# Kernel tuning notes

Hardware: AMD Instinct MI355X
Metric: run time of the kernel (lower is better)

The kernel has to match this reference:

```python
import jax, jax.numpy as jnp
import numpy as np

ALPHA = 4.0  # spikingjelly surrogate.Sigmoid default
TAU = 2.0    # LIFNode default

@jax.custom_vjp
def spike(x):
    return (x >= 0).astype(x.dtype)

def _spike_fwd(x):
    return spike(x), x

def _spike_bwd(x, g):
    s = jax.nn.sigmoid(ALPHA * x)
    return (g * ALPHA * s * (1.0 - s),)

spike.defvjp(_spike_fwd, _spike_bwd)

def lif(x_seq, v_th):
    # multi-step LIF over leading time dim; decay_input=True, v_reset=0 (hard reset)
    def step(v, x):
        v = v + (x - v) / TAU
        s = spike(v - v_th)
        return v * (1.0 - s), s
    _, s_seq = jax.lax.scan(step, jnp.zeros_like(x_seq[0]), x_seq)
    return s_seq

def bn_c(x, gamma, beta, mean, var, eps=1e-5):
    # eval-mode BatchNorm1d over channel axis 2 of [T,N,C,V]
    inv = (gamma / jnp.sqrt(var + eps))[None, None, :, None]
    return (x - mean[None, None, :, None]) * inv + beta[None, None, :, None]

def conv1x1(x, w):
    # 1x1 Conv1d == channel mixing: w [Cout,Cin], x [T,N,C,V]
    return jnp.einsum('oc,tncv->tnov', w, x)

def setup_inputs() -> dict:
    key = jax.random.key(0)
    T, N, C, V = 4, 512, 256, 25
    ks = jax.random.split(key, 24)
    def bn_params(k1, k2, k3, k4):
        return (jax.random.uniform(k1, (C,)) * 0.5 + 0.75,
                jax.random.normal(k2, (C,)) * 0.1,
                jax.random.normal(k3, (C,)) * 0.1,
                jax.random.uniform(k4, (C,)) * 0.5 + 0.5)
    x = jax.random.normal(ks[0], (T, N, C, V), dtype=jnp.float32)
    s = 1.0 / np.sqrt(C)
    wq = jax.random.normal(ks[1], (C, C)) * s
    wk = jax.random.normal(ks[2], (C, C)) * s
    wv = jax.random.normal(ks[3], (C, C)) * s
    wp = jax.random.normal(ks[4], (C, C)) * s
    bp = jax.random.normal(ks[5], (C,)) * 0.02
    qg, qb, qm, qvar = bn_params(ks[6], ks[7], ks[8], ks[9])
    kg, kb, km, kvar = bn_params(ks[10], ks[11], ks[12], ks[13])
    vg, vb, vm, vvar = bn_params(ks[14], ks[15], ks[16], ks[17])
    pg, pb, pm, pvar = bn_params(ks[18], ks[19], ks[20], ks[21])
    return dict(x=x, wq=wq, wk=wk, wv=wv, wp=wp, bp=bp,
                qg=qg, qb=qb, qm=qm, qvar=qvar,
                kg=kg, kb=kb, km=km, kvar=kvar,
                vg=vg, vb=vb, vm=vm, vvar=vvar,
                pg=pg, pb=pb, pm=pm, pvar=pvar)

def reference(x, wq, wk, wv, wp, bp, qg, qb, qm, qvar, kg, kb, km, kvar,
              vg, vb, vm, vvar, pg, pb, pm, pvar):
    T, N, C, V = x.shape
    H = 8
    D = C // H
    scale = 0.125

    def branch(w, g, b, m, var):
        s = lif(bn_c(conv1x1(x, w), g, b, m, var), 1.0)       # [T,N,C,V]
        # -> [T,N,V,C] -> [T,N,V,H,D] -> [T,N,H,V,D]
        return jnp.transpose(s, (0, 1, 3, 2)).reshape(T, N, V, H, D).transpose(0, 1, 3, 2, 4)

    q = branch(wq, qg, qb, qm, qvar)
    k = branch(wk, kg, kb, km, kvar)
    v = branch(wv, vg, vb, vm, vvar)

    attn = jnp.einsum('tnhvd,tnhwd->tnhvw', q, k)            # binary spike attn, no softmax
    y = jnp.einsum('tnhvw,tnhwd->tnhvd', attn, v) * scale    # [T,N,H,V,D]
    y = y.transpose(0, 1, 2, 4, 3).reshape(T, N, C, V)       # transpose(3,4) then merge H*D=C
    y = lif(y, 0.5)                                          # attn_lif, v_threshold=0.5
    y = conv1x1(y, wp) + bp[None, None, :, None]             # proj_conv (bias=True)
    y = lif(bn_c(y, pg, pb, pm, pvar), 1.0)                  # proj_bn + proj_lif
    return y + x                                             # residual
```

## Files before the change

### kernel.cpp

```cpp
#include <hip/hip_runtime.h>
#include <cstdint>
#include <cstddef>

#define T_ 4
#define N_ 512
#define C_ 256
#define V_ 25
#define H_ 8

typedef _Float16 half8_t __attribute__((ext_vector_type(8)));
typedef float f32x16 __attribute__((ext_vector_type(16)));

__device__ __forceinline__ f32x16 mfma16(half8_t a, half8_t b, f32x16 c) {
  return __builtin_amdgcn_mfma_f32_32x32x16_f16(a, b, c, 0, 0, 0);
}

__global__ void kw_stage(const float* __restrict__ wq, const float* __restrict__ wk,
                         const float* __restrict__ wv, const float* __restrict__ wp,
                         const float* __restrict__ qg, const float* __restrict__ qvar,
                         const float* __restrict__ kg, const float* __restrict__ kvar,
                         const float* __restrict__ vg, const float* __restrict__ vvar,
                         const float* __restrict__ pg, const float* __restrict__ pvar,
                         _Float16* __restrict__ Wstg) {
  int i = blockIdx.x * 512 + threadIdx.x;
  int j = i & 7, lane = (i >> 3) & 63, rt = (i >> 9) & 3, m = (i >> 11) & 1;
  int s = (i >> 12) & 3, p = (i >> 14) & 3, c = i >> 16;
  int kt = p * 4 + s;
  int row = rt * 32 + (lane & 31);
  int k = kt * 16 + (lane >> 5) * 8 + j;
  const float *w, *g, *va;
  int grow;
  if (c < 6) {
    int br = c >> 1;
    w = br == 0 ? wq : br == 1 ? wk : wv;
    g = br == 0 ? qg : br == 1 ? kg : vg;
    va = br == 0 ? qvar : br == 1 ? kvar : vvar;
    grow = (c & 1) * 128 + row;
  } else {
    w = wp; g = pg; va = pvar;
    grow = (c - 6) * 128 + row;
  }
  float sc = g[grow] / sqrtf(va[grow] + 1e-5f);
  float wv_ = w[grow * 256 + k] * sc;
  _Float16 hi = (_Float16)wv_;
  Wstg[i] = (m == 0) ? hi : (_Float16)(wv_ - (float)hi);
}

__global__ void kx_stage(const float* __restrict__ x, _Float16* __restrict__ X16) {
  __shared__ float Xt[256 * 28];
  const int n = blockIdx.x, tid = threadIdx.x;
  for (int t = 0; t < 4; ++t) {
    __syncthreads();
    for (int i = tid; i < 6400; i += 256) {
      int k = i / 25, v = i - k * 25;
      Xt[k * 28 + v] = x[(size_t)(t * N_ + n) * 6400 + i];
    }
    __syncthreads();
    for (int jj = tid; jj < 800; jj += 256) {
      int kt = jj / 50, r = jj - kt * 50;
      int v = r >> 1, lkg = r & 1;
      int k0 = kt * 16 + lkg * 8;
      half8_t hi, lo;
#pragma unroll
      for (int e = 0; e < 8; ++e) {
        float f = Xt[(k0 + e) * 28 + v];
        _Float16 h = (_Float16)f;
        hi[e] = h;
        lo[e] = (_Float16)(f - (float)h);
      }
      int col = v * 4 + t;
      size_t base = (size_t)(n * 2) * 25600 + kt * 1600 + col * 16 + lkg * 8;
      *(half8_t*)(X16 + base) = hi;
      *(half8_t*)(X16 + base + 25600) = lo;
    }
  }
}

#define STAGE_A(gidx, bufsel)                                                     \
  do {                                                                            \
    const _Float16* sp_ = Wstg + (size_t)(gidx) * 16384 + tid * 8;                \
    char* dp_ = Abuf + (bufsel) * 32768 + tid * 16;                               \
    __builtin_amdgcn_global_load_lds((const uint32_t*)(sp_),          (uint32_t*)(dp_),          16, 0, 0); \
    __builtin_amdgcn_global_load_lds((const uint32_t*)(sp_ + 4096),   (uint32_t*)(dp_ + 8192),   16, 0, 0); \
    __builtin_amdgcn_global_load_lds((const uint32_t*)(sp_ + 8192),   (uint32_t*)(dp_ + 16384),  16, 0, 0); \
    __builtin_amdgcn_global_load_lds((const uint32_t*)(sp_ + 12288),  (uint32_t*)(dp_ + 24576),  16, 0, 0); \
  } while (0)

#define MS_BYTE(colx, rowx) ((colx) * 256 + (((rowx) * 4) ^ (((colx) & 7) << 4)))

__global__ __launch_bounds__(512, 1) void k1d(
    const _Float16* __restrict__ X16, const _Float16* __restrict__ Wstg,
    const float* __restrict__ qg, const float* __restrict__ qb,
    const float* __restrict__ qm, const float* __restrict__ qvar,
    const float* __restrict__ kg, const float* __restrict__ kb,
    const float* __restrict__ km, const float* __restrict__ kvar,
    const float* __restrict__ vg, const float* __restrict__ vb,
    const float* __restrict__ vm, const float* __restrict__ vvar,
    uint32_t* __restrict__ masks) {
  __shared__ __align__(16) char LDSb[65536 + 51200 + 3072];
  char* Abuf = LDSb;
  char* MsB = LDSb + 65536;
  float* bicL = (float*)(LDSb + 65536 + 51200);

  const int np = blockIdx.x, tid = threadIdx.x;
  const int lane = tid & 63, wid = tid >> 6;
  const int rg = wid & 1, cg = wid >> 1;
  const int lr = lane & 31, lkg = lane >> 5;

  for (int i = tid; i < 768; i += 512) {
    int cc = i >> 7, row = i & 127;
    int br = cc >> 1, ch = (cc & 1) * 128 + row;
    const float* g  = br == 0 ? qg : br == 1 ? kg : vg;
    const float* be = br == 0 ? qb : br == 1 ? kb : vb;
    const float* mu = br == 0 ? qm : br == 1 ? km : vm;
    const float* va = br == 0 ? qvar : br == 1 ? kvar : vvar;
    float sc = g[ch] / sqrtf(va[ch] + 1e-5f);
    bicL[i] = be[ch] - mu[ch] * sc;
  }

  const int colw0 = cg * 64 + lr, colw1 = cg * 64 + 32 + lr;
  int c0 = colw0 > 199 ? 199 : colw0, c1 = colw1 > 199 ? 199 : colw1;
  int nl0 = (c0 >= 100), cl0 = c0 - nl0 * 100;
  int nl1 = (c1 >= 100), cl1 = c1 - nl1 * 100;
  const _Float16* xh0 = X16 + (size_t)((np * 2 + nl0) * 2 + 0) * 25600 + cl0 * 16 + lkg * 8;
  const _Float16* xl0 = X16 + (size_t)((np * 2 + nl0) * 2 + 1) * 25600 + cl0 * 16 + lkg * 8;
  const _Float16* xh1 = X16 + (size_t)((np * 2 + nl1) * 2 + 0) * 25600 + cl1 * 16 + lkg * 8;
  const _Float16* xl1 = X16 + (size_t)((np * 2 + nl1) * 2 + 1) * 25600 + cl1 * 16 + lkg * 8;

  STAGE_A(0, 0);
  half8_t Bh0[2], Bh1[2], Bl0[2], Bl1[2];
  Bh0[0] = *(const half8_t*)(xh0);
  Bh1[0] = *(const half8_t*)(xh1);
  Bl0[0] = *(const half8_t*)(xl0);
  Bl1[0] = *(const half8_t*)(xl1);

  for (int c = 0; c < 6; ++c) {
    const int br = c >> 1;
    f32x16 acc00 = {}, acc01 = {}, acc10 = {}, acc11 = {};
#pragma unroll
    for (int p = 0; p < 4; ++p) {
      __syncthreads();
      int gnext = c * 4 + p + 1;
      if (gnext < 24) STAGE_A(gnext, (p + 1) & 1);
#pragma unroll
      for (int s = 0; s < 4; ++s) {
        const int kt = p * 4 + s;
        const int cur = kt & 1, nxt = cur ^ 1;
        const int ktn = ((kt + 1) & 15) * 1600;
        Bh0[nxt] = *(const half8_t*)(xh0 + ktn);
        Bh1[nxt] = *(const half8_t*)(xh1 + ktn);
        Bl0[nxt] = *(const half8_t*)(xl0 + ktn);
        Bl1[nxt] = *(const half8_t*)(xl1 + ktn);
        const char* base = Abuf + (p & 1) * 32768 + s * 8192 + (rg * 2) * 1024 + lane * 16;
        half8_t Ah0 = *(const half8_t*)(base);
        half8_t Ah1 = *(const half8_t*)(base + 1024);
        half8_t Al0 = *(const half8_t*)(base + 4096);
        half8_t Al1 = *(const half8_t*)(base + 4096 + 1024);
        __builtin_amdgcn_s_setprio(1);
        acc00 = mfma16(Ah0, Bh0[cur], acc00);
        acc01 = mfma16(Ah0, Bh1[cur], acc01);
        acc10 = mfma16(Ah1, Bh0[cur], acc10);
        acc11 = mfma16(Ah1, Bh1[cur], acc11);
        acc00 = mfma16(Ah0, Bl0[cur], acc00);
        acc01 = mfma16(Ah0, Bl1[cur], acc01);
        acc10 = mfma16(Ah1, Bl0[cur], acc10);
        acc11 = mfma16(Ah1, Bl1[cur], acc11);
        acc00 = mfma16(Al0, Bh0[cur], acc00);
        acc01 = mfma16(Al0, Bh1[cur], acc01);
        acc10 = mfma16(Al1, Bh0[cur], acc10);
        acc11 = mfma16(Al1, Bh1[cur], acc11);
        __builtin_amdgcn_s_setprio(0);
      }
    }

#pragma unroll
    for (int pp = 0; pp < 2; ++pp) {
      __syncthreads();
      if (rg == pp) {
#pragma unroll
        for (int sub = 0; sub < 2; ++sub) {
#pragma unroll
          for (int ct = 0; ct < 2; ++ct) {
            int col = ct ? colw1 : colw0;
            if (col < 200) {
              f32x16 A = sub ? (ct ? acc11 : acc10) : (ct ? acc01 : acc00);
#pragma unroll
              for (int qq = 0; qq < 4; ++qq) {
                int rowb = sub * 32 + qq * 8 + lkg * 4;
                *(float4*)(MsB + MS_BYTE(col, rowb)) =
                    make_float4(A[qq * 4], A[qq * 4 + 1], A[qq * 4 + 2], A[qq * 4 + 3]);
              }
            }
          }
        }
      }
      __syncthreads();
      const int d = lane & 31, hl = lane >> 5;
      for (int it = 0; it < 7; ++it) {
        int task = it * 16 + wid * 2 + hl;
        bool valid = task < 100;
        int tnl = valid ? task / 50 : 0;
        int r = valid ? task - tnl * 50 : 0;
        int hgl = r / 25, v = r - (r / 25) * 25;
        int row = hgl * 32 + d;
        float bicv = bicL[c * 128 + pp * 64 + row];
        float st = 0.0f;
#pragma unroll
        for (int t = 0; t < 4; ++t) {
          int colx = tnl * 100 + v * 4 + t;
          float cu = *(const float*)(MsB + MS_BYTE(colx, row)) + bicv;
          st += (cu - st) * 0.5f;
          bool sb = valid && (st >= 1.0f);
          if (st >= 1.0f) st = 0.0f;
          unsigned long long b = __ballot(sb);
          if (valid && (lane == 0 || lane == 32)) {
            uint32_t wd = (lane == 0) ? (uint32_t)b : (uint32_t)(b >> 32);
            int hg = (c & 1) * 4 + pp * 2 + hgl;
            int n = np * 2 + tnl;
            masks[((((size_t)t * N_ + n) * 3 + br) * H_ + hg) * V_ + v] = wd;
          }
        }
      }
    }
  }
}

__launch_bounds__(64)
__global__ void k2_attn(const uint32_t* __restrict__ masks, uint32_t* __restrict__ mask2) {
  __shared__ uint32_t qs[T_][V_], ks_[T_][V_], vs[T_][V_];
  const int n = blockIdx.x >> 3;
  const int h = blockIdx.x & 7;
  const int l = threadIdx.x;
  for (int i = l; i < T_ * 3 * V_; i += 64) {
    int t = i / (3 * V_);
    int r = i - t * (3 * V_);
    int br = r / V_;
    int v = r - br * V_;
    uint32_t w = masks[(((size_t)t * N_ + n) * 3 + br) * (H_ * V_) + h * V_ + v];
    if (br == 0) qs[t][v] = w;
    else if (br == 1) ks_[t][v] = w;
    else vs[t][v] = w;
  }
  __syncthreads();
  const int hi = l >> 5, d = l & 31;
  float st[13];
#pragma unroll
  for (int vv = 0; vv < 13; ++vv) st[vv] = 0.0f;
#pragma unroll
  for (int t = 0; t < 4; ++t) {
    uint32_t q[13];
    int y[13];
#pragma unroll
    for (int vv = 0; vv < 13; ++vv) {
      int v = vv * 2 + hi;
      q[vv] = qs[t][v < V_ ? v : 0];
      y[vv] = 0;
    }
    for (int w = 0; w < V_; ++w) {
      uint32_t kw = ks_[t][w];
      int vb = (int)((vs[t][w] >> d) & 1u);
#pragma unroll
      for (int vv = 0; vv < 13; ++vv) y[vv] += __popc(q[vv] & kw) * vb;
    }
#pragma unroll
    for (int vv = 0; vv < 13; ++vv) {
      int v = vv * 2 + hi;
      bool valid = (v < V_);
      float yf = 0.125f * (float)y[vv];
      st[vv] += (yf - st[vv]) * 0.5f;
      bool s = valid && (st[vv] >= 0.5f);
      if (st[vv] >= 0.5f) st[vv] = 0.0f;
      unsigned long long b = __ballot(s);
      if (valid && (l == 0 || l == 32)) {
        uint32_t wd = (l == 0) ? (uint32_t)b : (uint32_t)(b >> 32);
        mask2[(((size_t)t * N_ + n) * V_ + v) * H_ + h] = wd;
      }
    }
  }
}

__global__ __launch_bounds__(512, 1) void k3d(
    const float* __restrict__ x, const _Float16* __restrict__ Wstg,
    const uint32_t* __restrict__ mask2, const float* __restrict__ bp,
    const float* __restrict__ pg, const float* __restrict__ pb,
    const float* __restrict__ pm, const float* __restrict__ pvar,
    float* __restrict__ out) {
  __shared__ __align__(16) char LDSb[65536 + 51200 + 1024 + 6400];
  char* Abuf = LDSb;
  char* MsB = LDSb + 65536;
  float* bicL = (float*)(LDSb + 65536 + 51200);
  uint32_t* m2s = (uint32_t*)(LDSb + 65536 + 51200 + 1024);

  const int np = blockIdx.x, tid = threadIdx.x;
  const int lane = tid & 63, wid = tid >> 6;
  const int rg = wid & 1, cg = wid >> 1;
  const int lr = lane & 31, lkg = lane >> 5;

  for (int i = tid; i < 1600; i += 512) {
    int nl = i / 800, j = i - nl * 800;
    int t = j / 200, r = j - t * 200;
    m2s[i] = mask2[(size_t)(t * N_ + np * 2 + nl) * 200 + r];
  }
  if (tid < 256) {
    float sc = pg[tid] / sqrtf(pvar[tid] + 1e-5f);
    bicL[tid] = fmaf(bp[tid] - pm[tid], sc, pb[tid]);
  }
  __syncthreads();

  const int colw0 = cg * 64 + lr, colw1 = cg * 64 + 32 + lr;
  int c0 = colw0 > 199 ? 199 : colw0, c1 = colw1 > 199 ? 199 : colw1;
  int nl0 = (c0 >= 100), cl0 = c0 - nl0 * 100;
  int nl1 = (c1 >= 100), cl1 = c1 - nl1 * 100;
  const int v0 = cl0 >> 2, t0 = cl0 & 3, v1 = cl1 >> 2, t1 = cl1 & 3;
  const int mb0 = nl0 * 800 + t0 * 200 + v0 * 8;
  const int mb1 = nl1 * 800 + t1 * 200 + v1 * 8;

  STAGE_A(24, 0);
  for (int c = 0; c < 2; ++c) {
    f32x16 acc00 = {}, acc01 = {}, acc10 = {}, acc11 = {};
#pragma unroll
    for (int p = 0; p < 4; ++p) {
      __syncthreads();
      int gnext = 24 + c * 4 + p + 1;
      if (gnext < 32) STAGE_A(gnext, (p + 1) & 1);
#pragma unroll
      for (int s = 0; s < 4; ++s) {
        const int kt = p * 4 + s;
        uint32_t w0 = m2s[mb0 + (kt >> 1)];
        uint32_t w1 = m2s[mb1 + (kt >> 1)];
        int sh = (kt & 1) * 16 + lkg * 8;
        half8_t B0, B1;
#pragma unroll
        for (int jj = 0; jj < 8; ++jj) {
          B0[jj] = ((w0 >> (sh + jj)) & 1u) ? (_Float16)1.0f : (_Float16)0.0f;
          B1[jj] = ((w1 >> (sh + jj)) & 1u) ? (_Float16)1.0f : (_Float16)0.0f;
        }
        const char* base = Abuf + (p & 1) * 32768 + s * 8192 + (rg * 2) * 1024 + lane * 16;
        half8_t Ah0 = *(const half8_t*)(base);
        half8_t Ah1 = *(const half8_t*)(base + 1024);
        half8_t Al0 = *(const half8_t*)(base + 4096);
        half8_t Al1 = *(const half8_t*)(base + 4096 + 1024);
        __builtin_amdgcn_s_setprio(1);
        acc00 = mfma16(Ah0, B0, acc00);
        acc01 = mfma16(Ah0, B1, acc01);
        acc10 = mfma16(Ah1, B0, acc10);
        acc11 = mfma16(Ah1, B1, acc11);
        acc00 = mfma16(Al0, B0, acc00);
        acc01 = mfma16(Al0, B1, acc01);
        acc10 = mfma16(Al1, B0, acc10);
        acc11 = mfma16(Al1, B1, acc11);
        __builtin_amdgcn_s_setprio(0);
      }
    }

#pragma unroll
    for (int pp = 0; pp < 2; ++pp) {
      __syncthreads();
      if (rg == pp) {
#pragma unroll
        for (int sub = 0; sub < 2; ++sub) {
#pragma unroll
          for (int ct = 0; ct < 2; ++ct) {
            int col = ct ? colw1 : colw0;
            if (col < 200) {
              f32x16 A = sub ? (ct ? acc11 : acc10) : (ct ? acc01 : acc00);
#pragma unroll
              for (int qq = 0; qq < 4; ++qq) {
                int rowb = sub * 32 + qq * 8 + lkg * 4;
                *(float4*)(MsB + MS_BYTE(col, rowb)) =
                    make_float4(A[qq * 4], A[qq * 4 + 1], A[qq * 4 + 2], A[qq * 4 + 3]);
              }
            }
          }
        }
      }
      __syncthreads();
      {
        const int d = lane & 31, hl = lane >> 5;
        for (int it = 0; it < 7; ++it) {
          int task = it * 16 + wid * 2 + hl;
          bool valid = task < 100;
          int tnl = valid ? task / 50 : 0;
          int r = valid ? task - tnl * 50 : 0;
          int hgl = r / 25, v = r - (r / 25) * 25;
          int row = hgl * 32 + d;
          float bicv = bicL[c * 128 + pp * 64 + row];
          float st = 0.0f;
#pragma unroll
          for (int t = 0; t < 4; ++t) {
            int colx = tnl * 100 + v * 4 + t;
            char* mp = MsB + MS_BYTE(colx, row);
            if (valid) {
              float cu = *(const float*)(mp) + bicv;
              st += (cu - st) * 0.5f;
              float sv = (st >= 1.0f) ? 1.0f : 0.0f;
              if (st >= 1.0f) st = 0.0f;
              *(float*)(mp) = sv;
            }
          }
        }
      }
      __syncthreads();
      for (int ii = tid; ii < 12800; ii += 512) {
        int t = ii / 3200, r = ii - t * 3200;
        int nl = r / 1600, r2 = r - nl * 1600;
        int cl = r2 / 25, v = r2 - cl * 25;
        int colx = nl * 100 + v * 4 + t;
        float sv = *(const float*)(MsB + MS_BYTE(colx, cl));
        size_t go = (size_t)(t * N_ + np * 2 + nl) * 6400 +
                    (size_t)(c * 128 + pp * 64 + cl) * 25 + v;
        out[go] = sv + x[go];
      }
    }
  }
}

extern "C" void kernel_launch(void* const* d_in, const int* in_sizes, int n_in,
                              void* d_out, int out_size, void* d_ws, size_t ws_size,
                              hipStream_t stream) {
  const float* x    = (const float*)d_in[0];
  const float* wq   = (const float*)d_in[1];
  const float* wk   = (const float*)d_in[2];
  const float* wv   = (const float*)d_in[3];
  const float* wp   = (const float*)d_in[4];
  const float* bp   = (const float*)d_in[5];
  const float* qg   = (const float*)d_in[6];
  const float* qb   = (const float*)d_in[7];
  const float* qm   = (const float*)d_in[8];
  const float* qvar = (const float*)d_in[9];
  const float* kg   = (const float*)d_in[10];
  const float* kb   = (const float*)d_in[11];
  const float* km   = (const float*)d_in[12];
  const float* kvar = (const float*)d_in[13];
  const float* vg   = (const float*)d_in[14];
  const float* vb   = (const float*)d_in[15];
  const float* vm   = (const float*)d_in[16];
  const float* vvar = (const float*)d_in[17];
  const float* pg   = (const float*)d_in[18];
  const float* pb   = (const float*)d_in[19];
  const float* pm   = (const float*)d_in[20];
  const float* pvar = (const float*)d_in[21];

  _Float16* Wstg = (_Float16*)d_ws;
  _Float16* X16  = (_Float16*)d_ws + 524288;
  uint32_t* masks = (uint32_t*)((char*)d_ws + 1048576 + 52428800);
  uint32_t* mask2 = masks + 1228800;

  kw_stage<<<1024, 512, 0, stream>>>(wq, wk, wv, wp, qg, qvar, kg, kvar,
                                     vg, vvar, pg, pvar, Wstg);
  kx_stage<<<512, 256, 0, stream>>>(x, X16);
  k1d<<<256, 512, 0, stream>>>(X16, Wstg, qg, qb, qm, qvar, kg, kb, km, kvar,
                               vg, vb, vm, vvar, masks);
  k2_attn<<<4096, 64, 0, stream>>>(masks, mask2);
  k3d<<<256, 512, 0, stream>>>(x, Wstg, mask2, bp, pg, pb, pm, pvar, (float*)d_out);
}
```

Before: 316.8 us.

## Compute LIF spikes in registers via cross-lane permutes instead of LDS staging

```diff
diff --git a/kernel.cpp b/kernel.cpp
--- a/kernel.cpp
+++ b/kernel.cpp
@@ -88,7 +88,7 @@
 
 #define MS_BYTE(colx, rowx) ((colx) * 256 + (((rowx) * 4) ^ (((colx) & 7) << 4)))
 
-__global__ __launch_bounds__(512, 1) void k1d(
+__global__ __launch_bounds__(512, 4) void k1d(
     const _Float16* __restrict__ X16, const _Float16* __restrict__ Wstg,
     const float* __restrict__ qg, const float* __restrict__ qb,
     const float* __restrict__ qm, const float* __restrict__ qvar,
@@ -97,10 +97,9 @@
     const float* __restrict__ vg, const float* __restrict__ vb,
     const float* __restrict__ vm, const float* __restrict__ vvar,
     uint32_t* __restrict__ masks) {
-  __shared__ __align__(16) char LDSb[65536 + 51200 + 3072];
+  __shared__ __align__(16) char LDSb[65536 + 3072];
   char* Abuf = LDSb;
-  char* MsB = LDSb + 65536;
-  float* bicL = (float*)(LDSb + 65536 + 51200);
+  float* bicL = (float*)(LDSb + 65536);
 
   const int np = blockIdx.x, tid = threadIdx.x;
   const int lane = tid & 63, wid = tid >> 6;
@@ -133,6 +132,7 @@
   Bh1[0] = *(const half8_t*)(xh1);
   Bl0[0] = *(const half8_t*)(xl0);
   Bl1[0] = *(const half8_t*)(xl1);
+  __syncthreads();
 
   for (int c = 0; c < 6; ++c) {
     const int br = c >> 1;
@@ -173,51 +173,38 @@
       }
     }
 
-#pragma unroll
-    for (int pp = 0; pp < 2; ++pp) {
-      __syncthreads();
-      if (rg == pp) {
-#pragma unroll
-        for (int sub = 0; sub < 2; ++sub) {
-#pragma unroll
-          for (int ct = 0; ct < 2; ++ct) {
-            int col = ct ? colw1 : colw0;
-            if (col < 200) {
-              f32x16 A = sub ? (ct ? acc11 : acc10) : (ct ? acc01 : acc00);
-#pragma unroll
-              for (int qq = 0; qq < 4; ++qq) {
-                int rowb = sub * 32 + qq * 8 + lkg * 4;
-                *(float4*)(MsB + MS_BYTE(col, rowb)) =
-                    make_float4(A[qq * 4], A[qq * 4 + 1], A[qq * 4 + 2], A[qq * 4 + 3]);
-              }
+    {
+      const int tq = lane & 3;
+#pragma unroll
+      for (int hl = 0; hl < 2; ++hl) {
+#pragma unroll
+        for (int ct = 0; ct < 2; ++ct) {
+          f32x16 A = hl ? (ct ? acc11 : acc10) : (ct ? acc01 : acc00);
+          int col = ct ? colw1 : colw0;
+          bool valid = col < 200;
+          int tnl = (col >= 100) ? 1 : 0;
+          int v = (col >> 2) - tnl * 25;
+          uint32_t word = 0;
+#pragma unroll
+          for (int rr = 0; rr < 16; ++rr) {
+            int rowc = (rr & 3) + 8 * (rr >> 2) + 4 * lkg;
+            float m = A[rr] + bicL[c * 128 + (2 * rg + hl) * 32 + rowc];
+            float st = 0.0f;
+#pragma unroll
+            for (int p = 0; p < 4; ++p) {
+              float mp = __int_as_float(__builtin_amdgcn_ds_bpermute(
+                  ((lane & ~3) + p) << 2, __float_as_int(m)));
+              st += (mp - st) * 0.5f;
+              bool sb = st >= 1.0f;
+              if (sb) st = 0.0f;
+              if (sb && p == tq) word |= (1u << rowc);
             }
           }
-        }
-      }
-      __syncthreads();
-      const int d = lane & 31, hl = lane >> 5;
-      for (int it = 0; it < 7; ++it) {
-        int task = it * 16 + wid * 2 + hl;
-        bool valid = task < 100;
-        int tnl = valid ? task / 50 : 0;
-        int r = valid ? task - tnl * 50 : 0;
-        int hgl = r / 25, v = r - (r / 25) * 25;
-        int row = hgl * 32 + d;
-        float bicv = bicL[c * 128 + pp * 64 + row];
-        float st = 0.0f;
-#pragma unroll
-        for (int t = 0; t < 4; ++t) {
-          int colx = tnl * 100 + v * 4 + t;
-          float cu = *(const float*)(MsB + MS_BYTE(colx, row)) + bicv;
-          st += (cu - st) * 0.5f;
-          bool sb = valid && (st >= 1.0f);
-          if (st >= 1.0f) st = 0.0f;
-          unsigned long long b = __ballot(sb);
-          if (valid && (lane == 0 || lane == 32)) {
-            uint32_t wd = (lane == 0) ? (uint32_t)b : (uint32_t)(b >> 32);
-            int hg = (c & 1) * 4 + pp * 2 + hgl;
+          word |= __shfl_xor(word, 32);
+          if (valid && lkg == 0) {
+            int hg = (c & 1) * 4 + rg * 2 + hl;
             int n = np * 2 + tnl;
-            masks[((((size_t)t * N_ + n) * 3 + br) * H_ + hg) * V_ + v] = wd;
+            masks[((((size_t)tq * N_ + n) * 3 + br) * H_ + hg) * V_ + v] = word;
           }
         }
       }
```

Result: slower. 358.9 us (+13.3%).
